# Kernel optimization log

Measured on AMD Instinct MI355X. Metric: run time of the kernel, lower is better.

Reference implementation:

```python
import jax, jax.numpy as jnp
import numpy as np

B, L, H, O, C = 64, 32, 128, 16384, 32


def setup_inputs() -> dict:
    key = jax.random.key(0)
    ks = jax.random.split(key, 8)
    s = lambda k, shp, fan: jax.random.normal(k, shp, jnp.float32) / np.sqrt(fan)
    return {
        "z": jax.random.normal(ks[0], (B, L), jnp.float32),
        "feature_embedding": jax.random.normal(ks[1], (O, C), jnp.float32),
        "feature_bias": jax.random.normal(ks[2], (O, 1), jnp.float32),
        "Wz": s(ks[3], (L, H), L),
        "bz": jnp.zeros((H,), jnp.float32),
        "W1": s(ks[4], (H + C + 1, H), H + C + 1),
        "b1": jnp.zeros((H,), jnp.float32),
        "W2": s(ks[5], (H, 1), H),
        "b2": jnp.zeros((1,), jnp.float32),
    }


def reference(z, feature_embedding, feature_bias, Wz, bz, W1, b1, W2, b2):
    # z_processor: Linear + ReLU (dropout_rate=0)
    pz = jax.nn.relu(z @ Wz + bz)  # [B, H]
    # concat([pz, F, b], -1) @ W1  ==  pz@W1_h + F@W1_f + b*W1_b  (no [B,O,H+C+1] materialization)
    W1_h, W1_f, W1_b = W1[:H], W1[H:H + C], W1[H + C:]  # [H,H],[C,H],[1,H]
    h = jax.nn.relu(
        (pz @ W1_h)[:, None, :]                    # [B,1,H]
        + (feature_embedding @ W1_f)[None, :, :]   # [1,O,H]
        + feature_bias * W1_b                      # [O,H] broadcast
        + b1
    )  # [B, O, H]
    out = jnp.einsum("boh,ho->bo", h, W2) + b2  # [B, O]
    return out
```

## Files before the change

### kernel.cpp

```cpp
#include <hip/hip_runtime.h>

#define Bb 64
#define Ll 32
#define Hh 128
#define Oo 16384
#define Cc 32
#define TOo 64
#define NT 1024

__global__ __launch_bounds__(256) void prep_kernel(
    const float* __restrict__ z, const float* __restrict__ Wz,
    const float* __restrict__ bz, const float* __restrict__ W1,
    const float* __restrict__ W2,
    float* __restrict__ A, float* __restrict__ SA2w)
{
    __shared__ float pz[2][Hh];
    __shared__ float ps[2][Hh];
    const int t  = threadIdx.x;
    const int h  = t & (Hh - 1);
    const int bb = t >> 7;
    const int b  = blockIdx.x * 2 + bb;

    float v = bz[h];
#pragma unroll
    for (int c = 0; c < Ll; ++c)
        v = fmaf(z[b * Ll + c], Wz[c * Hh + h], v);
    pz[bb][h] = fmaxf(v, 0.f);
    __syncthreads();

    float a = 0.f;
#pragma unroll
    for (int k = 0; k < Hh; ++k)
        a = fmaf(pz[bb][k], W1[k * Hh + h], a);
    A[b * Hh + h] = a;
    ps[bb][h] = 0.5f * W2[h] * a;
    __syncthreads();

    if (h == 0) {
        float s = 0.f;
        for (int k = 0; k < Hh; ++k) s += ps[bb][k];
        SA2w[b] = s;
    }
}

__global__ __launch_bounds__(NT) void main_kernel(
    const float* __restrict__ A,  const float* __restrict__ SA2w,
    const float* __restrict__ fe, const float* __restrict__ fb,
    const float* __restrict__ W1, const float* __restrict__ b1,
    const float* __restrict__ W2, const float* __restrict__ b2,
    float* __restrict__ out)
{
    __shared__ float fe_s[TOo][Cc];
    __shared__ float gT[Hh][TOo + 1];
    __shared__ float A_s[Bb][Hh];
    __shared__ float part[4][Bb][TOo];
    __shared__ float w2_s[Hh];
    __shared__ float fb_s[TOo];

    const int t  = threadIdx.x;
    const int o0 = blockIdx.x * TOo;

    if (t < 512) ((float4*)fe_s)[t] = ((const float4*)(fe + o0 * Cc))[t];
    ((float4*)A_s)[t]        = ((const float4*)A)[t];
    ((float4*)A_s)[t + 1024] = ((const float4*)A)[t + 1024];
    if (t < Hh)  w2_s[t] = 0.5f * W2[t];
    if (t < TOo) fb_s[t] = fb[o0 + t];
    const float b2v = b2[0];
    __syncthreads();

    {
        const int h  = t & 127;
        const int og = t >> 7;
        float w1f[Cc];
#pragma unroll
        for (int c = 0; c < Cc; ++c)
            w1f[c] = W1[(Hh + c) * Hh + h];
        const float w1b = W1[(Hh + Cc) * Hh + h];
        const float b1h = b1[h];
#pragma unroll
        for (int j = 0; j < 8; ++j) {
            const int o = og * 8 + j;
            float g = fmaf(fb_s[o], w1b, b1h);
#pragma unroll
            for (int cc = 0; cc < Cc / 4; ++cc) {
                const float4 f4 = ((const float4*)fe_s[o])[cc];
                g = fmaf(f4.x, w1f[4 * cc + 0], g);
                g = fmaf(f4.y, w1f[4 * cc + 1], g);
                g = fmaf(f4.z, w1f[4 * cc + 2], g);
                g = fmaf(f4.w, w1f[4 * cc + 3], g);
            }
            gT[h][o] = g;
        }
    }
    __syncthreads();

    const int lane = t & 63;
    const int wave = __builtin_amdgcn_readfirstlane(t >> 6);
    const int hh   = wave & 3;
    const int bg   = wave >> 2;
    const int h0   = hh * 32;
    const int b0   = bg * 16;

    float gv[32];
#pragma unroll
    for (int k = 0; k < 32; ++k)
        gv[k] = gT[h0 + k][lane];

    float w2v[32];
#pragma unroll
    for (int k = 0; k < 8; ++k) {
        const float4 w4 = ((const float4*)(w2_s + h0))[k];
        w2v[4 * k + 0] = w4.x; w2v[4 * k + 1] = w4.y;
        w2v[4 * k + 2] = w4.z; w2v[4 * k + 3] = w4.w;
    }

    float sg = 0.f;
#pragma unroll
    for (int k = 0; k < 32; ++k)
        sg = fmaf(w2v[k], gv[k], sg);

    float acc[16];
#pragma unroll
    for (int bi = 0; bi < 16; ++bi) acc[bi] = sg;

#pragma unroll
    for (int jc = 0; jc < 8; ++jc) {
#pragma unroll
        for (int bi = 0; bi < 16; ++bi) {
            const float4 a4 = *(const float4*)&A_s[b0 + bi][h0 + 4 * jc];
            acc[bi] = fmaf(__builtin_fabsf(a4.x + gv[4 * jc + 0]), w2v[4 * jc + 0], acc[bi]);
            acc[bi] = fmaf(__builtin_fabsf(a4.y + gv[4 * jc + 1]), w2v[4 * jc + 1], acc[bi]);
            acc[bi] = fmaf(__builtin_fabsf(a4.z + gv[4 * jc + 2]), w2v[4 * jc + 2], acc[bi]);
            acc[bi] = fmaf(__builtin_fabsf(a4.w + gv[4 * jc + 3]), w2v[4 * jc + 3], acc[bi]);
        }
    }

#pragma unroll
    for (int bi = 0; bi < 16; ++bi)
        part[hh][b0 + bi][lane] = acc[bi];
    __syncthreads();

#pragma unroll
    for (int q = 0; q < 4; ++q) {
        const int b = wave * 4 + q;
        const float r = part[0][b][lane] + part[1][b][lane]
                      + part[2][b][lane] + part[3][b][lane];
        out[b * Oo + o0 + lane] = r + SA2w[b] + b2v;
    }
}

extern "C" void kernel_launch(void* const* d_in, const int* in_sizes, int n_in,
                              void* d_out, int out_size, void* d_ws, size_t ws_size,
                              hipStream_t stream) {
    (void)in_sizes; (void)n_in; (void)out_size; (void)ws_size;
    const float* z   = (const float*)d_in[0];
    const float* fe  = (const float*)d_in[1];
    const float* fb  = (const float*)d_in[2];
    const float* Wz  = (const float*)d_in[3];
    const float* bz  = (const float*)d_in[4];
    const float* W1  = (const float*)d_in[5];
    const float* b1  = (const float*)d_in[6];
    const float* W2  = (const float*)d_in[7];
    const float* b2  = (const float*)d_in[8];
    float* out  = (float*)d_out;
    float* A    = (float*)d_ws;
    float* SA2w = A + Bb * Hh;

    prep_kernel<<<Bb / 2, 256, 0, stream>>>(z, Wz, bz, W1, W2, A, SA2w);
    main_kernel<<<Oo / TOo, NT, 0, stream>>>(A, SA2w, fe, fb, W1, b1, W2, b2, out);
}
```

Baseline: 87.15 us.

## Replace shared-memory staging of A, fe, W2 with register loads and readlane broadcasts

Drops the LDS staging buffers for A, the feature embedding tile, W2 and feature_bias, along with the sync that followed them. Each wave now loads its own slice of these into registers and shares the values across lanes with v_readlane into scalar registers. This cuts LDS traffic and shared-memory footprint and removes one barrier. The cost is that every readlane is a separate scalar instruction in the inner loops, which may add instruction overhead and latency.

```diff
diff --git a/kernel.cpp b/kernel.cpp
--- a/kernel.cpp
+++ b/kernel.cpp
@@ -7,6 +7,10 @@
 #define Cc 32
 #define TOo 64
 #define NT 1024
+
+__device__ __forceinline__ float rdlane(float v, int l) {
+    return __int_as_float(__builtin_amdgcn_readlane(__float_as_int(v), l));
+}
 
 __global__ __launch_bounds__(256) void prep_kernel(
     const float* __restrict__ z, const float* __restrict__ Wz,
@@ -50,69 +54,61 @@
     const float* __restrict__ W2, const float* __restrict__ b2,
     float* __restrict__ out)
 {
-    __shared__ float fe_s[TOo][Cc];
     __shared__ float gT[Hh][TOo + 1];
-    __shared__ float A_s[Bb][Hh];
     __shared__ float part[4][Bb][TOo];
-    __shared__ float w2_s[Hh];
-    __shared__ float fb_s[TOo];
 
-    const int t  = threadIdx.x;
-    const int o0 = blockIdx.x * TOo;
+    const int t    = threadIdx.x;
+    const int o0   = blockIdx.x * TOo;
+    const int lane = t & 63;
+    const int wave = __builtin_amdgcn_readfirstlane(t >> 6);
 
-    if (t < 512) ((float4*)fe_s)[t] = ((const float4*)(fe + o0 * Cc))[t];
-    ((float4*)A_s)[t]        = ((const float4*)A)[t];
-    ((float4*)A_s)[t + 1024] = ((const float4*)A)[t + 1024];
-    if (t < Hh)  w2_s[t] = 0.5f * W2[t];
-    if (t < TOo) fb_s[t] = fb[o0 + t];
-    const float b2v = b2[0];
-    __syncthreads();
+    const int hh = wave & 3, bg = wave >> 2;
+    const int h0 = hh * 32,  b0 = bg * 16;
+
+    const int bi_l = lane >> 2, hc_l = lane & 3;
+    const float* Ap = A + (b0 + bi_l) * Hh + h0 + hc_l * 8;
+    const float4 av_lo = *(const float4*)(Ap);
+    const float4 av_hi = *(const float4*)(Ap + 4);
 
     {
-        const int h  = t & 127;
-        const int og = t >> 7;
+        const int hG = ((wave & 1) << 6) + lane;
+        const int og = wave >> 1;
+        const int ol = lane >> 3, ccl = lane & 7;
+        const float4 fe4 = *(const float4*)(fe + (o0 + og * 8 + ol) * Cc + ccl * 4);
+
         float w1f[Cc];
 #pragma unroll
         for (int c = 0; c < Cc; ++c)
-            w1f[c] = W1[(Hh + c) * Hh + h];
-        const float w1b = W1[(Hh + Cc) * Hh + h];
-        const float b1h = b1[h];
+            w1f[c] = W1[(Hh + c) * Hh + hG];
+        const float w1b = W1[(Hh + Cc) * Hh + hG];
+        const float b1h = b1[hG];
+
 #pragma unroll
         for (int j = 0; j < 8; ++j) {
-            const int o = og * 8 + j;
-            float g = fmaf(fb_s[o], w1b, b1h);
+            float g = fmaf(fb[o0 + og * 8 + j], w1b, b1h);
 #pragma unroll
-            for (int cc = 0; cc < Cc / 4; ++cc) {
-                const float4 f4 = ((const float4*)fe_s[o])[cc];
-                g = fmaf(f4.x, w1f[4 * cc + 0], g);
-                g = fmaf(f4.y, w1f[4 * cc + 1], g);
-                g = fmaf(f4.z, w1f[4 * cc + 2], g);
-                g = fmaf(f4.w, w1f[4 * cc + 3], g);
+            for (int c2 = 0; c2 < 8; ++c2) {
+                const int L = j * 8 + c2;
+                g = fmaf(rdlane(fe4.x, L), w1f[c2 * 4 + 0], g);
+                g = fmaf(rdlane(fe4.y, L), w1f[c2 * 4 + 1], g);
+                g = fmaf(rdlane(fe4.z, L), w1f[c2 * 4 + 2], g);
+                g = fmaf(rdlane(fe4.w, L), w1f[c2 * 4 + 3], g);
             }
-            gT[h][o] = g;
+            gT[hG][og * 8 + j] = g;
         }
     }
     __syncthreads();
-
-    const int lane = t & 63;
-    const int wave = __builtin_amdgcn_readfirstlane(t >> 6);
-    const int hh   = wave & 3;
-    const int bg   = wave >> 2;
-    const int h0   = hh * 32;
-    const int b0   = bg * 16;
 
     float gv[32];
 #pragma unroll
     for (int k = 0; k < 32; ++k)
         gv[k] = gT[h0 + k][lane];
 
+    const float w2l = 0.5f * W2[h0 + (lane & 31)];
     float w2v[32];
 #pragma unroll
-    for (int k = 0; k < 8; ++k) {
-        const float4 w4 = ((const float4*)(w2_s + h0))[k];
-        w2v[4 * k + 0] = w4.x; w2v[4 * k + 1] = w4.y;
-        w2v[4 * k + 2] = w4.z; w2v[4 * k + 3] = w4.w;
-    }
+    for (int k = 0; k < 32; ++k)
+        w2v[k] = rdlane(w2l, k);
 
     float sg = 0.f;
 #pragma unroll
@@ -125,13 +121,18 @@
 
 #pragma unroll
     for (int jc = 0; jc < 8; ++jc) {
+        const float4 a4s = (jc & 1) ? av_hi : av_lo;
+        const float g0 = gv[4 * jc + 0], g1 = gv[4 * jc + 1];
+        const float g2 = gv[4 * jc + 2], g3 = gv[4 * jc + 3];
+        const float u0 = w2v[4 * jc + 0], u1 = w2v[4 * jc + 1];
+        const float u2 = w2v[4 * jc + 2], u3 = w2v[4 * jc + 3];
 #pragma unroll
         for (int bi = 0; bi < 16; ++bi) {
-            const float4 a4 = *(const float4*)&A_s[b0 + bi][h0 + 4 * jc];
-            acc[bi] = fmaf(__builtin_fabsf(a4.x + gv[4 * jc + 0]), w2v[4 * jc + 0], acc[bi]);
-            acc[bi] = fmaf(__builtin_fabsf(a4.y + gv[4 * jc + 1]), w2v[4 * jc + 1], acc[bi]);
-            acc[bi] = fmaf(__builtin_fabsf(a4.z + gv[4 * jc + 2]), w2v[4 * jc + 2], acc[bi]);
-            acc[bi] = fmaf(__builtin_fabsf(a4.w + gv[4 * jc + 3]), w2v[4 * jc + 3], acc[bi]);
+            const int L = bi * 4 + (jc >> 1);
+            acc[bi] = fmaf(__builtin_fabsf(rdlane(a4s.x, L) + g0), u0, acc[bi]);
+            acc[bi] = fmaf(__builtin_fabsf(rdlane(a4s.y, L) + g1), u1, acc[bi]);
+            acc[bi] = fmaf(__builtin_fabsf(rdlane(a4s.z, L) + g2), u2, acc[bi]);
+            acc[bi] = fmaf(__builtin_fabsf(rdlane(a4s.w, L) + g3), u3, acc[bi]);
         }
     }
 
@@ -140,6 +141,7 @@
         part[hh][b0 + bi][lane] = acc[bi];
     __syncthreads();
 
+    const float b2v = b2[0];
 #pragma unroll
     for (int q = 0; q < 4; ++q) {
         const int b = wave * 4 + q;
```

Measured after the change: 92.21 us. 5.8% more time.
